# Optimization experiments

Measured on AMD Instinct MI355X. Metric: run time of the kernel, lower is better.

## Reference

```python
import jax, jax.numpy as jnp
import numpy as np

ROPE_DIMS = 16
NUM_HEADS = 16
NUM_KV_HEADS = 4
HEAD_DIM = 128
ROPE_BASE = 10000.0


def _rope_cos_sin(T, dtype):
    # inv_freq over rope_dims=16 -> 8 freqs; emb = cat(freqs, freqs) -> 16 cols
    inv_freq = 1.0 / (ROPE_BASE ** (jnp.arange(0, ROPE_DIMS, 2, dtype=jnp.float32) / ROPE_DIMS))
    t = jnp.arange(T, dtype=jnp.float32)
    freqs = jnp.outer(t, inv_freq)              # [T, 8]
    emb = jnp.concatenate([freqs, freqs], -1)   # [T, 16]
    return jnp.cos(emb).astype(dtype), jnp.sin(emb).astype(dtype)


def _apply_rotary(x):
    # x: [B, H, T, head_dim]; rotate only first ROPE_DIMS dims
    T = x.shape[-2]
    cos, sin = _rope_cos_sin(T, x.dtype)        # [T, 16]
    x_rope, x_pass = x[..., :ROPE_DIMS], x[..., ROPE_DIMS:]
    half = ROPE_DIMS // 2
    x1, x2 = x_rope[..., :half], x_rope[..., half:]
    rotated = jnp.concatenate([-x2, x1], -1)
    x_rope = x_rope * cos + rotated * sin
    return jnp.concatenate([x_rope, x_pass], -1)


def setup_inputs() -> dict:
    key = jax.random.key(0)
    ks = jax.random.split(key, 5)
    B, T, C = 4, 2048, 2048
    kv_out = NUM_KV_HEADS * HEAD_DIM
    s = 0.02
    return {
        "x_normed": jax.random.normal(ks[0], (B, T, C), jnp.float32),
        "q_w": jax.random.normal(ks[1], (C, C), jnp.float32) * s,
        "k_w": jax.random.normal(ks[2], (kv_out, C), jnp.float32) * s,
        "v_w": jax.random.normal(ks[3], (kv_out, C), jnp.float32) * s,
        "out_w": jax.random.normal(ks[4], (C, C), jnp.float32) * s,
        "qk_gain": jnp.ones((1, NUM_HEADS, 1, 1), jnp.float32),
    }


def reference(x_normed, q_w, k_w, v_w, out_w, qk_gain):
    B, T, C = x_normed.shape
    H, kvH, hd = NUM_HEADS, NUM_KV_HEADS, HEAD_DIM
    q = (x_normed @ q_w.T).reshape(B, T, H, hd).transpose(0, 2, 1, 3)    # [B,H,T,hd]
    k = (x_normed @ k_w.T).reshape(B, T, kvH, hd).transpose(0, 2, 1, 3)  # [B,kvH,T,hd]
    v = (x_normed @ v_w.T).reshape(B, T, kvH, hd).transpose(0, 2, 1, 3)
    q = _apply_rotary(q)
    k = _apply_rotary(k)
    q = q * qk_gain
    reps = H // kvH
    if reps > 1:
        k = jnp.repeat(k, reps, axis=1)  # [B,H,T,hd]
        v = jnp.repeat(v, reps, axis=1)
    scale = 1.0 / jnp.sqrt(jnp.asarray(hd, q.dtype))
    scores = jnp.einsum('bhqd,bhkd->bhqk', q, k) * scale
    causal = jnp.tril(jnp.ones((T, T), bool))
    scores = jnp.where(causal, scores, jnp.asarray(-jnp.inf, scores.dtype))
    probs = jax.nn.softmax(scores, axis=-1)
    attn = jnp.einsum('bhqk,bhkd->bhqd', probs, v)
    attn = attn.transpose(0, 2, 1, 3).reshape(B, T, C)
    out = attn @ out_w.T
    return out, v[:, :kvH]
```

## Files before the change

kernel.cpp:

```cpp
#include <hip/hip_runtime.h>
#include <hip/hip_bf16.h>
#include <stdint.h>
#include <math.h>

#define T_SEQ 2048
#define CDIM  2048
#define NB    4
#define NH    16
#define NKV   4
#define HD    128

typedef __attribute__((ext_vector_type(8))) short short8;
typedef __attribute__((ext_vector_type(4))) float f32x4;

__device__ __forceinline__ void gload_lds16(const void* g, void* l) {
  __builtin_amdgcn_global_load_lds((const __attribute__((address_space(1))) void*)g,
                                   (__attribute__((address_space(3))) void*)l, 16, 0, 0);
}

__device__ __forceinline__ f32x4 mfma_bf16(short8 a, short8 b, f32x4 c) {
  return __builtin_amdgcn_mfma_f32_16x16x32_bf16(a, b, c, 0, 0, 0);
}

__device__ __forceinline__ unsigned short f2bf(float x) {
  union { float f; unsigned u; } v; v.f = x;
  unsigned r = v.u + 0x7fffu + ((v.u >> 16) & 1u);
  return (unsigned short)(r >> 16);
}

__device__ __forceinline__ unsigned pk_bf16(float a, float b) {
  unsigned r;
  asm("v_cvt_pk_bf16_f32 %0, %1, %2" : "=v"(r) : "v"(a), "v"(b));
  return r;
}

__device__ __forceinline__ float exp2_fast(float x) {
  float r;
  asm("v_exp_f32 %0, %1" : "=v"(r) : "v"(x));
  return r;
}

__global__ void cvt_all(const float* __restrict__ x,  const float* __restrict__ qw,
                        const float* __restrict__ kw, const float* __restrict__ vw,
                        const float* __restrict__ ow,
                        unsigned short* __restrict__ xb,  unsigned short* __restrict__ qwb,
                        unsigned short* __restrict__ kwb, unsigned short* __restrict__ vwb,
                        unsigned short* __restrict__ owb) {
  const int bid = blockIdx.x;
  const float* src; unsigned short* dst; int base, nb, n4;
  if (bid < 2048)      { src = x;  dst = xb;  base = 0;    nb = 2048; n4 = 4194304; }
  else if (bid < 2560) { src = qw; dst = qwb; base = 2048; nb = 512;  n4 = 1048576; }
  else if (bid < 2688) { src = kw; dst = kwb; base = 2560; nb = 128;  n4 = 262144;  }
  else if (bid < 2816) { src = vw; dst = vwb; base = 2688; nb = 128;  n4 = 262144;  }
  else                 { src = ow; dst = owb; base = 2816; nb = 512;  n4 = 1048576; }
  const int stride = nb * 256;
  for (int i = (bid - base) * 256 + threadIdx.x; i < n4; i += stride) {
    float4 v = *(const float4*)(src + (size_t)i * 4);
    ushort4 o;
    o.x = f2bf(v.x); o.y = f2bf(v.y); o.z = f2bf(v.z); o.w = f2bf(v.w);
    *(ushort4*)(dst + (size_t)i * 4) = o;
  }
}

__global__ void transpose_v(const unsigned short* __restrict__ V,
                            unsigned short* __restrict__ Vt) {
  __shared__ unsigned short tile[64][72];
  const int tb = blockIdx.x * 64;
  const int db = blockIdx.y * 64;
  const int g  = blockIdx.z;
  const unsigned short* src = V  + (size_t)g * T_SEQ * HD;
  unsigned short*       dst = Vt + (size_t)g * T_SEQ * HD;
#pragma unroll
  for (int i = 0; i < 2; ++i) {
    int s = threadIdx.x + i * 256;
    int t = s >> 3, c = s & 7;
    short8 vv = *(const short8*)(src + (size_t)(tb + t) * HD + db + c * 8);
#pragma unroll
    for (int j = 0; j < 8; ++j) tile[c * 8 + j][t] = (unsigned short)vv[j];
  }
  __syncthreads();
#pragma unroll
  for (int i = 0; i < 2; ++i) {
    int s = threadIdx.x + i * 256;
    int d = s >> 3, c = s & 7;
    short8 o = *(const short8*)(&tile[d][c * 8]);
    *(short8*)(dst + (size_t)(db + d) * T_SEQ + tb + c * 8) = o;
  }
}

template<int MODE>
__launch_bounds__(256, 2)
__global__ void gemm_bt(const unsigned short* __restrict__ A,
                        const unsigned short* __restrict__ W,
                        int N, int K,
                        unsigned short* __restrict__ obf,
                        float* __restrict__ of32,
                        const float* __restrict__ gain)
{
  __shared__ alignas(16) short As[128 * 64];
  __shared__ alignas(16) short Bs[128 * 64];
  const int tid = threadIdx.x;
  const int lane = tid & 63, w = tid >> 6;
  const int wr = w >> 1, wc = w & 1;
  const int lr = lane & 15, lg = lane >> 4;

  const int nwg  = gridDim.x * gridDim.y;
  const int orig = blockIdx.y * gridDim.x + blockIdx.x;
  const int cpx  = nwg >> 3;
  const int swz  = (orig & 7) * cpx + (orig >> 3);
  const int m0 = (swz / gridDim.x) * 128, n0 = (swz % gridDim.x) * 128;

  f32x4 acc[4][4] = {};

  const int nkt = K >> 6;
  for (int kt = 0; kt < nkt; ++kt) {
    __syncthreads();
#pragma unroll
    for (int q = 0; q < 4; ++q) {
      int s = (w * 4 + q) * 64 + lane;
      int row = s >> 3;
      int cs2 = (s & 7) ^ (row & 7);
      gload_lds16(A + (size_t)(m0 + row) * K + (kt << 6) + cs2 * 8,
                  (char*)As + (w * 4 + q) * 1024);
      gload_lds16(W + (size_t)(n0 + row) * K + (kt << 6) + cs2 * 8,
                  (char*)Bs + (w * 4 + q) * 1024);
    }
    __syncthreads();
#pragma unroll
    for (int ks = 0; ks < 2; ++ks) {
      short8 af[4], bfr[4];
#pragma unroll
      for (int i = 0; i < 4; ++i) {
        int ra = wr * 64 + i * 16 + lr;
        int rb = wc * 64 + i * 16 + lr;
        af[i]  = *(const short8*)(As + ra * 64 + (((ks * 4 + lg) ^ (ra & 7)) << 3));
        bfr[i] = *(const short8*)(Bs + rb * 64 + (((ks * 4 + lg) ^ (rb & 7)) << 3));
      }
#pragma unroll
      for (int i = 0; i < 4; ++i)
#pragma unroll
        for (int j = 0; j < 4; ++j)
          acc[i][j] = mfma_bf16(af[i], bfr[j], acc[i][j]);
    }
  }

  const size_t VOFF = (size_t)NB * NKV * T_SEQ * HD;

#pragma unroll
  for (int i = 0; i < 4; ++i) {
    const int mbase = m0 + wr * 64 + i * 16 + lg * 4;
#pragma unroll
    for (int j = 0; j < 4; ++j) {
      const int ncol = n0 + wc * 64 + j * 16 + lr;
      if constexpr (MODE == 0) {
#pragma unroll
        for (int r = 0; r < 4; ++r)
          of32[(size_t)(mbase + r) * N + ncol] = acc[i][j][r];
      } else {
        const int hh = ncol >> 7;
        const int d  = ncol & 127;
        const bool rope = (d < 16) && (MODE == 1 || hh < 4);
#pragma unroll
        for (int r = 0; r < 4; ++r) {
          float val = acc[i][j][r];
          const int m  = mbase + r;
          const int t  = m & (T_SEQ - 1);
          const int bb = m >> 11;
          if (rope) {
            float partner = __shfl_xor(val, 8);
            float invf = exp2f(-(float)(d & 7) * 1.6609640474436813f);
            float ang = (float)t * invf;
            float sn, cn;
            sincosf(ang, &sn, &cn);
            float rot = (d < 8) ? -partner : partner;
            val = val * cn + rot * sn;
          }
          if constexpr (MODE == 1) {
            val *= gain[hh] * 0.12751742676f;
            obf[(size_t)((bb * NH + hh) * T_SEQ + t) * HD + d] = f2bf(val);
          } else if constexpr (MODE == 4) {
            if (hh < 4) {
              obf[(size_t)((bb * NKV + hh) * T_SEQ + t) * HD + d] = f2bf(val);
            } else {
              size_t idx = (size_t)((bb * NKV + (hh - 4)) * T_SEQ + t) * HD + d;
              obf[VOFF + idx] = f2bf(val);
              if (hh == 4) {
#pragma unroll
                for (int rep = 0; rep < NKV; ++rep)
                  of32[(size_t)((bb * NKV + rep) * T_SEQ + t) * HD + d] = val;
              }
            }
          }
        }
      }
    }
  }
}

__launch_bounds__(512, 4)
__global__ void attn_fwd(const unsigned short* __restrict__ Q,
                         const unsigned short* __restrict__ Kg,
                         const unsigned short* __restrict__ Vt,
                         unsigned short* __restrict__ O)
{
  __shared__ alignas(16) short Ks[2][64 * 128];
  __shared__ alignas(16) short Vs[2][128 * 64];
  __shared__ alignas(16) short Ps[128 * 64];

  const int pairi = blockIdx.x;
  const int h = blockIdx.y, b = blockIdx.z;
  const int kvh = h >> 2;
  const int tid = threadIdx.x, lane = tid & 63, w = tid >> 6;
  const int lr = lane & 15, lg = lane >> 4;

  const unsigned short* Qb  = Q  + ((size_t)(b * NH  + h)   * T_SEQ) * HD;
  const unsigned short* Kb  = Kg + ((size_t)(b * NKV + kvh) * T_SEQ) * HD;
  const unsigned short* Vtb = Vt + ((size_t)(b * NKV + kvh) * HD) * T_SEQ;

  auto stageK = [&](int kt, int buf) {
#pragma unroll
    for (int i = 0; i < 2; ++i) {
      int s = tid + i * 512;
      int row = s >> 4, c = s & 15, cs = c ^ (row & 7);
      gload_lds16(Kb + (size_t)(kt * 64 + row) * HD + cs * 8,
                  (char*)&Ks[buf][0] + w * 1024 + i * 8192);
    }
  };
  auto stageV = [&](int kt, int buf) {
#pragma unroll
    for (int i = 0; i < 2; ++i) {
      int s = tid + i * 512;
      int row = s >> 3, c = s & 7, cs = c ^ (row & 7);
      gload_lds16(Vtb + (size_t)row * T_SEQ + kt * 64 + cs * 8,
                  (char*)&Vs[buf][0] + w * 1024 + i * 8192);
    }
  };

  auto run_seg = [&](int qtile) {
    const int q0 = qtile * 128;
    const int rw = q0 + w * 16;
    const int qg = rw + lr;
    const int dtile = rw >> 6;

    short8 qf[4];
#pragma unroll
    for (int ks = 0; ks < 4; ++ks)
      qf[ks] = *(const short8*)(Qb + (size_t)qg * HD + ks * 32 + lg * 8);

    f32x4 acc_o[8] = {};
    float mrow = 0.0f;
    float lrow = 0.0f;

    const int nkt = (qtile + 1) * 2;

    stageK(0, 0);
    stageV(0, 0);
    asm volatile("s_waitcnt vmcnt(2)" ::: "memory");
    __builtin_amdgcn_s_barrier();
    int cur = 0;

    for (int kt = 0; kt < nkt; ++kt) {
      const int tn = (kt + 1 < nkt) ? kt + 1 : kt;
      stageK(tn, cur ^ 1);

      const bool active = (kt <= dtile);
      if (active) {
        const short* KL = &Ks[cur][0];
        f32x4 acc2[4] = {};
        __builtin_amdgcn_s_setprio(1);
#pragma unroll
        for (int kb = 0; kb < 4; ++kb) {
          int key = kb * 16 + lr;
#pragma unroll
          for (int ks = 0; ks < 4; ++ks) {
            short8 kf = *(const short8*)(KL + key * 128 + (((ks * 4 + lg) ^ (key & 7)) << 3));
            acc2[kb] = mfma_bf16(kf, qf[ks], acc2[kb]);
          }
        }
        __builtin_amdgcn_s_setprio(0);

        const bool needmask = (kt == dtile);
        float pmax = -3.0e38f;
#pragma unroll
        for (int kb = 0; kb < 4; ++kb)
#pragma unroll
          for (int r = 0; r < 4; ++r) {
            float sv = acc2[kb][r];
            if (needmask && (kt * 64 + kb * 16 + lg * 4 + r > qg)) sv = -3.0e38f;
            acc2[kb][r] = sv;
            pmax = fmaxf(pmax, sv);
          }
        pmax = fmaxf(pmax, __shfl_xor(pmax, 16));
        pmax = fmaxf(pmax, __shfl_xor(pmax, 32));

        if (!__all(pmax - mrow <= 11.0f)) {
          float mn = fmaxf(mrow, pmax);
          float al = exp2_fast(mrow - mn);
          mrow = mn;
          lrow *= al;
#pragma unroll
          for (int db = 0; db < 8; ++db)
#pragma unroll
            for (int r = 0; r < 4; ++r) acc_o[db][r] *= al;
        }

        float s0 = 0.f;
#pragma unroll
        for (int kb = 0; kb < 4; ++kb) {
          float p0 = exp2_fast(acc2[kb][0] - mrow);
          float p1 = exp2_fast(acc2[kb][1] - mrow);
          float p2 = exp2_fast(acc2[kb][2] - mrow);
          float p3 = exp2_fast(acc2[kb][3] - mrow);
          s0 += (p0 + p1) + (p2 + p3);
          uint2 w2;
          w2.x = pk_bf16(p0, p1);
          w2.y = pk_bf16(p2, p3);
          int cc = (kb * 2 + (lg >> 1)) ^ (lr & 7);
          *(uint2*)(Ps + (w * 16 + lr) * 64 + (cc << 3) + ((lg & 1) << 2)) = w2;
        }
        s0 += __shfl_xor(s0, 16);
        s0 += __shfl_xor(s0, 32);
        lrow += s0;
      }

      stageV(tn, cur ^ 1);
      asm volatile("s_waitcnt vmcnt(4)" ::: "memory");
      __builtin_amdgcn_s_barrier();

      if (active) {
        const short* VL = &Vs[cur][0];
        const int qq = w * 16 + lr;
        short8 pf0 = *(const short8*)(Ps + qq * 64 + (((0 + lg) ^ (lr & 7)) << 3));
        short8 pf1 = *(const short8*)(Ps + qq * 64 + (((4 + lg) ^ (lr & 7)) << 3));
        __builtin_amdgcn_s_setprio(1);
#pragma unroll
        for (int db = 0; db < 8; ++db) {
          int vrow = db * 16 + lr;
          short8 v0 = *(const short8*)(VL + vrow * 64 + (((0 + lg) ^ (vrow & 7)) << 3));
          short8 v1 = *(const short8*)(VL + vrow * 64 + (((4 + lg) ^ (vrow & 7)) << 3));
          acc_o[db] = mfma_bf16(v0, pf0, acc_o[db]);
          acc_o[db] = mfma_bf16(v1, pf1, acc_o[db]);
        }
        __builtin_amdgcn_s_setprio(0);
      }

      asm volatile("s_waitcnt vmcnt(2)" ::: "memory");
      __builtin_amdgcn_s_barrier();
      cur ^= 1;
    }

    asm volatile("s_waitcnt vmcnt(0)" ::: "memory");
    __builtin_amdgcn_s_barrier();

    float invl = 1.0f / lrow;
#pragma unroll
    for (int db = 0; db < 8; ++db) {
      uint2 o2;
      o2.x = pk_bf16(acc_o[db][0] * invl, acc_o[db][1] * invl);
      o2.y = pk_bf16(acc_o[db][2] * invl, acc_o[db][3] * invl);
      *(uint2*)(O + (size_t)(b * T_SEQ + qg) * CDIM + h * HD + db * 16 + lg * 4) = o2;
    }
  };

  run_seg(15 - pairi);
  run_seg(pairi);
}

extern "C" void kernel_launch(void* const* d_in, const int* in_sizes, int n_in,
                              void* d_out, int out_size, void* d_ws, size_t ws_size,
                              hipStream_t stream) {
  (void)in_sizes; (void)n_in; (void)out_size; (void)ws_size;
  const float* x    = (const float*)d_in[0];
  const float* qw   = (const float*)d_in[1];
  const float* kw   = (const float*)d_in[2];
  const float* vw   = (const float*)d_in[3];
  const float* ow   = (const float*)d_in[4];
  const float* gain = (const float*)d_in[5];
  float* out  = (float*)d_out;
  float* vout = out + (size_t)NB * T_SEQ * CDIM;

  char* ws = (char*)d_ws;
  unsigned short* xb  = (unsigned short*)(ws);
  unsigned short* Qb  = (unsigned short*)(ws + 33554432);
  unsigned short* Kb  = (unsigned short*)(ws + 67108864);
  unsigned short* Vb  = (unsigned short*)(ws + 75497472);
  unsigned short* qwb = (unsigned short*)(ws + 83886080);
  unsigned short* kwb = (unsigned short*)(ws + 92274688);
  unsigned short* vwb = (unsigned short*)(ws + 94371840);
  unsigned short* owb = (unsigned short*)(ws + 96468992);
  unsigned short* Ab  = xb;
  unsigned short* Vtb = qwb;

  cvt_all<<<3328, 256, 0, stream>>>(x, qw, kw, vw, ow, xb, qwb, kwb, vwb, owb);

  gemm_bt<1><<<dim3(16, 64), 256, 0, stream>>>(xb, qwb, CDIM, CDIM, Qb, nullptr, gain);
  gemm_bt<4><<<dim3(8,  64), 256, 0, stream>>>(xb, kwb, 2 * NKV * HD, CDIM, Kb, vout, nullptr);

  transpose_v<<<dim3(T_SEQ / 64, HD / 64, NB * NKV), 256, 0, stream>>>(Vb, Vtb);

  attn_fwd<<<dim3(8, 16, 4), 512, 0, stream>>>(Qb, Kb, Vtb, Ab);

  gemm_bt<0><<<dim3(16, 64), 256, 0, stream>>>(Ab, owb, CDIM, CDIM, nullptr, out, nullptr);
}
```

Baseline: 337.1 us.

## Add 256x256-tile double-buffered GEMM for Q and output projections

Adds a new 512-thread GEMM kernel with 256x256 output tiles, double-buffered LDS staging through direct global-to-LDS loads, and MFMA phases interleaved with the next tile's loads and priority hints. The Q projection and output projection now use it in place of the 128x128 kernel, which raises data reuse per loaded byte and overlaps memory with compute. The K/V GEMM keeps the old kernel, which is trimmed to the only mode still in use. The larger tile gives fewer workgroups (256 for a 256-CU part), which risks lower occupancy and heavier register pressure with 32 accumulators per lane.

```diff
diff --git a/kernel.cpp b/kernel.cpp
--- a/kernel.cpp
+++ b/kernel.cpp
@@ -89,6 +89,142 @@
 }
 
 template<int MODE>
+__launch_bounds__(512, 2)
+__global__ void gemm256(const unsigned short* __restrict__ A,
+                        const unsigned short* __restrict__ W,
+                        int N, int K,
+                        unsigned short* __restrict__ obf,
+                        float* __restrict__ of32,
+                        const float* __restrict__ gain)
+{
+  __shared__ alignas(16) short As[2][2][256 * 32];
+  __shared__ alignas(16) short Bs[2][2][256 * 32];
+  const int tid = threadIdx.x;
+  const int lane = tid & 63, w = tid >> 6;
+  const int wr = w >> 2, wc = w & 3;
+  const int lr = lane & 15, lg = lane >> 4;
+
+  const int nwg  = gridDim.x * gridDim.y;
+  const int orig = blockIdx.y * gridDim.x + blockIdx.x;
+  const int cpx  = nwg >> 3;
+  const int swz  = (orig & 7) * cpx + (orig >> 3);
+  const int m0 = (swz / gridDim.x) * 256, n0 = (swz % gridDim.x) * 256;
+
+  f32x4 acc[8][4] = {};
+  const int nkt = K >> 6;
+  const int rsw = (lr >> 1) & 3;
+
+  auto stageA = [&](int kt, int buf, int kk) {
+#pragma unroll
+    for (int i = 0; i < 2; ++i) {
+      int t = i * 512 + tid;
+      int row = t >> 2;
+      int cs = (t & 3) ^ ((t >> 3) & 3);
+      gload_lds16(A + (size_t)(m0 + row) * K + kt * 64 + kk * 32 + cs * 8,
+                  (char*)&As[buf][kk][0] + i * 8192 + w * 1024);
+    }
+  };
+  auto stageB = [&](int kt, int buf, int kk) {
+#pragma unroll
+    for (int i = 0; i < 2; ++i) {
+      int t = i * 512 + tid;
+      int row = t >> 2;
+      int cs = (t & 3) ^ ((t >> 3) & 3);
+      gload_lds16(W + (size_t)(n0 + row) * K + kt * 64 + kk * 32 + cs * 8,
+                  (char*)&Bs[buf][kk][0] + i * 8192 + w * 1024);
+    }
+  };
+
+  stageA(0, 0, 0); stageB(0, 0, 0); stageA(0, 0, 1); stageB(0, 0, 1);
+  asm volatile("s_waitcnt vmcnt(4)" ::: "memory");
+  __builtin_amdgcn_s_barrier();
+
+  int cur = 0;
+  for (int kt = 0; kt < nkt; ++kt) {
+    const int tn = (kt + 1 < nkt) ? kt + 1 : kt;
+#pragma unroll
+    for (int kk = 0; kk < 2; ++kk) {
+      short8 bfr[4], af[4];
+#pragma unroll
+      for (int fn = 0; fn < 4; ++fn) {
+        int rb = wc * 64 + fn * 16 + lr;
+        bfr[fn] = *(const short8*)((const char*)&Bs[cur][kk][0] + rb * 64 + ((lg ^ rsw) << 4));
+      }
+#pragma unroll
+      for (int fm = 0; fm < 4; ++fm) {
+        int ra = wr * 128 + fm * 16 + lr;
+        af[fm] = *(const short8*)((const char*)&As[cur][kk][0] + ra * 64 + ((lg ^ rsw) << 4));
+      }
+      stageA(tn, cur ^ 1, kk);
+      __builtin_amdgcn_s_barrier();
+      __builtin_amdgcn_s_setprio(1);
+#pragma unroll
+      for (int fm = 0; fm < 4; ++fm)
+#pragma unroll
+        for (int fn = 0; fn < 4; ++fn)
+          acc[fm][fn] = mfma_bf16(af[fm], bfr[fn], acc[fm][fn]);
+      __builtin_amdgcn_s_setprio(0);
+      __builtin_amdgcn_s_barrier();
+
+#pragma unroll
+      for (int fm = 0; fm < 4; ++fm) {
+        int ra = wr * 128 + (4 + fm) * 16 + lr;
+        af[fm] = *(const short8*)((const char*)&As[cur][kk][0] + ra * 64 + ((lg ^ rsw) << 4));
+      }
+      stageB(tn, cur ^ 1, kk);
+      asm volatile("s_waitcnt vmcnt(4)" ::: "memory");
+      __builtin_amdgcn_s_barrier();
+      __builtin_amdgcn_s_setprio(1);
+#pragma unroll
+      for (int fm = 0; fm < 4; ++fm)
+#pragma unroll
+        for (int fn = 0; fn < 4; ++fn)
+          acc[4 + fm][fn] = mfma_bf16(af[fm], bfr[fn], acc[4 + fm][fn]);
+      __builtin_amdgcn_s_setprio(0);
+      __builtin_amdgcn_s_barrier();
+    }
+    cur ^= 1;
+  }
+  asm volatile("s_waitcnt vmcnt(0)" ::: "memory");
+
+#pragma unroll
+  for (int fm = 0; fm < 8; ++fm) {
+    const int mbase = m0 + wr * 128 + fm * 16 + lg * 4;
+#pragma unroll
+    for (int fn = 0; fn < 4; ++fn) {
+      const int ncol = n0 + wc * 64 + fn * 16 + lr;
+      if constexpr (MODE == 0) {
+#pragma unroll
+        for (int r = 0; r < 4; ++r)
+          of32[(size_t)(mbase + r) * N + ncol] = acc[fm][fn][r];
+      } else {
+        const int hh = ncol >> 7;
+        const int d  = ncol & 127;
+        const bool rope = ((wc & 1) == 0) && (fn == 0);
+#pragma unroll
+        for (int r = 0; r < 4; ++r) {
+          float val = acc[fm][fn][r];
+          const int m  = mbase + r;
+          const int t  = m & (T_SEQ - 1);
+          const int bb = m >> 11;
+          if (rope) {
+            float partner = __shfl_xor(val, 8);
+            float invf = exp2f(-(float)(d & 7) * 1.6609640474436813f);
+            float ang = (float)t * invf;
+            float sn, cn;
+            sincosf(ang, &sn, &cn);
+            float rot = (d < 8) ? -partner : partner;
+            val = val * cn + rot * sn;
+          }
+          val *= gain[hh] * 0.12751742676f;
+          obf[(size_t)((bb * NH + hh) * T_SEQ + t) * HD + d] = f2bf(val);
+        }
+      }
+    }
+  }
+}
+
+template<int MODE>
 __launch_bounds__(256, 2)
 __global__ void gemm_bt(const unsigned short* __restrict__ A,
                         const unsigned short* __restrict__ W,
@@ -152,44 +288,33 @@
 #pragma unroll
     for (int j = 0; j < 4; ++j) {
       const int ncol = n0 + wc * 64 + j * 16 + lr;
-      if constexpr (MODE == 0) {
-#pragma unroll
-        for (int r = 0; r < 4; ++r)
-          of32[(size_t)(mbase + r) * N + ncol] = acc[i][j][r];
-      } else {
-        const int hh = ncol >> 7;
-        const int d  = ncol & 127;
-        const bool rope = (d < 16) && (MODE == 1 || hh < 4);
-#pragma unroll
-        for (int r = 0; r < 4; ++r) {
-          float val = acc[i][j][r];
-          const int m  = mbase + r;
-          const int t  = m & (T_SEQ - 1);
-          const int bb = m >> 11;
-          if (rope) {
-            float partner = __shfl_xor(val, 8);
-            float invf = exp2f(-(float)(d & 7) * 1.6609640474436813f);
-            float ang = (float)t * invf;
-            float sn, cn;
-            sincosf(ang, &sn, &cn);
-            float rot = (d < 8) ? -partner : partner;
-            val = val * cn + rot * sn;
-          }
-          if constexpr (MODE == 1) {
-            val *= gain[hh] * 0.12751742676f;
-            obf[(size_t)((bb * NH + hh) * T_SEQ + t) * HD + d] = f2bf(val);
-          } else if constexpr (MODE == 4) {
-            if (hh < 4) {
-              obf[(size_t)((bb * NKV + hh) * T_SEQ + t) * HD + d] = f2bf(val);
-            } else {
-              size_t idx = (size_t)((bb * NKV + (hh - 4)) * T_SEQ + t) * HD + d;
-              obf[VOFF + idx] = f2bf(val);
-              if (hh == 4) {
-#pragma unroll
-                for (int rep = 0; rep < NKV; ++rep)
-                  of32[(size_t)((bb * NKV + rep) * T_SEQ + t) * HD + d] = val;
-              }
-            }
+      const int hh = ncol >> 7;
+      const int d  = ncol & 127;
+      const bool rope = (d < 16) && (hh < 4);
+#pragma unroll
+      for (int r = 0; r < 4; ++r) {
+        float val = acc[i][j][r];
+        const int m  = mbase + r;
+        const int t  = m & (T_SEQ - 1);
+        const int bb = m >> 11;
+        if (rope) {
+          float partner = __shfl_xor(val, 8);
+          float invf = exp2f(-(float)(d & 7) * 1.6609640474436813f);
+          float ang = (float)t * invf;
+          float sn, cn;
+          sincosf(ang, &sn, &cn);
+          float rot = (d < 8) ? -partner : partner;
+          val = val * cn + rot * sn;
+        }
+        if (hh < 4) {
+          obf[(size_t)((bb * NKV + hh) * T_SEQ + t) * HD + d] = f2bf(val);
+        } else {
+          size_t idx = (size_t)((bb * NKV + (hh - 4)) * T_SEQ + t) * HD + d;
+          obf[VOFF + idx] = f2bf(val);
+          if (hh == 4) {
+#pragma unroll
+            for (int rep = 0; rep < NKV; ++rep)
+              of32[(size_t)((bb * NKV + rep) * T_SEQ + t) * HD + d] = val;
           }
         }
       }
@@ -393,12 +518,12 @@
 
   cvt_all<<<3328, 256, 0, stream>>>(x, qw, kw, vw, ow, xb, qwb, kwb, vwb, owb);
 
-  gemm_bt<1><<<dim3(16, 64), 256, 0, stream>>>(xb, qwb, CDIM, CDIM, Qb, nullptr, gain);
-  gemm_bt<4><<<dim3(8,  64), 256, 0, stream>>>(xb, kwb, 2 * NKV * HD, CDIM, Kb, vout, nullptr);
+  gemm256<1><<<dim3(8, 32), 512, 0, stream>>>(xb, qwb, CDIM, CDIM, Qb, nullptr, gain);
+  gemm_bt<4><<<dim3(8, 64), 256, 0, stream>>>(xb, kwb, 2 * NKV * HD, CDIM, Kb, vout, nullptr);
 
   transpose_v<<<dim3(T_SEQ / 64, HD / 64, NB * NKV), 256, 0, stream>>>(Vb, Vtb);
 
   attn_fwd<<<dim3(8, 16, 4), 512, 0, stream>>>(Qb, Kb, Vtb, Ab);
 
-  gemm_bt<0><<<dim3(16, 64), 256, 0, stream>>>(Ab, owb, CDIM, CDIM, nullptr, out, nullptr);
-}
+  gemm256<0><<<dim3(8, 32), 512, 0, stream>>>(Ab, owb, CDIM, CDIM, nullptr, out, nullptr);
+}
```

After: 320.4 us. -4.9%, faster.
